# Performance work log

Hardware: AMD Instinct MI355X
Metric: run time of the kernel (lower is better)

The kernel has to match this reference:

```python
import jax, jax.numpy as jnp
import numpy as np

N_AGENTS, N_ENEMIES, N_ACTIONS = 8, 8, 14
ALLY_F, ENEMY_F = 8, 6
EMBED, RNN, HYPEMB, HYPHID = 32, 64, 64, 64
STATE_DIM = N_AGENTS * ALLY_F + N_ENEMIES * ENEMY_F + N_AGENTS * N_ACTIONS  # 224


def setup_inputs() -> dict:
    key = jax.random.key(0)
    ks = jax.random.split(key, 16)
    b, t = 64, 256
    rn = lambda k, s, sc=0.05: jax.random.normal(k, s, jnp.float32) * sc
    return dict(
        qvals=rn(ks[0], (b, t, N_AGENTS), 1.0),
        states=rn(ks[1], (b, t, STATE_DIM), 1.0),
        hidden_states=rn(ks[2], (b, t, N_AGENTS, RNN), 1.0),
        hw1_w=rn(ks[3], (RNN, EMBED)), hw1_b=jnp.zeros((EMBED,), jnp.float32),
        en_h1w=rn(ks[4], (ENEMY_F, HYPHID)), en_h1b=jnp.zeros((HYPHID,), jnp.float32),
        en_h2w=rn(ks[5], (HYPHID, ENEMY_F * HYPEMB)), en_h2b=jnp.zeros((ENEMY_F * HYPEMB,), jnp.float32),
        en_bias=jnp.zeros((1, HYPEMB), jnp.float32),
        al_h1w=rn(ks[6], (ALLY_F, HYPHID)), al_h1b=jnp.zeros((HYPHID,), jnp.float32),
        al_h2w=rn(ks[7], (HYPHID, ALLY_F * HYPEMB)), al_h2b=jnp.zeros((ALLY_F * HYPEMB,), jnp.float32),
        al_bias=jnp.zeros((1, HYPEMB), jnp.float32),
        act_w=rn(ks[8], (N_ACTIONS, HYPEMB)), act_b=jnp.zeros((HYPEMB,), jnp.float32),
        hb1_w=rn(ks[9], (HYPEMB, EMBED)), hb1_b=jnp.zeros((EMBED,), jnp.float32),
        hw2_w=rn(ks[10], (HYPEMB, EMBED)), hw2_b=jnp.zeros((EMBED,), jnp.float32),
        hb2_w=rn(ks[11], (HYPEMB, 1)), hb2_b=jnp.zeros((1,), jnp.float32),
    )


def _hyperlinear(x, h1w, h1b, h2w, h2b, bias, din, dout):
    # hypernet MLP -> per-sample weight matrix [rows, din, dout]
    h = jax.nn.relu(x @ h1w + h1b)
    W = (h @ h2w + h2b).reshape(-1, din, dout)
    return jnp.einsum('bi,bio->bo', x, W) + bias


def reference(qvals, states, hidden_states, hw1_w, hw1_b,
              en_h1w, en_h1b, en_h2w, en_h2b, en_bias,
              al_h1w, al_h1b, al_h2w, al_h2b, al_bias,
              act_w, act_b, hb1_w, hb1_b, hw2_w, hw2_b, hb2_w, hb2_b):
    b, t, _ = qvals.shape
    BT = b * t
    s = states.reshape(BT, STATE_DIM)
    ally = s[:, :N_AGENTS * ALLY_F].reshape(-1, ALLY_F)                # [BT*A, 8]
    enemy = s[:, N_AGENTS * ALLY_F:N_AGENTS * ALLY_F + N_ENEMIES * ENEMY_F].reshape(-1, ENEMY_F)
    actions = s[:, N_AGENTS * ALLY_F + N_ENEMIES * ENEMY_F:].reshape(BT, N_AGENTS, N_ACTIONS)

    embed_ally = _hyperlinear(ally, al_h1w, al_h1b, al_h2w, al_h2b, al_bias,
                              ALLY_F, HYPEMB).reshape(BT, N_AGENTS, HYPEMB).mean(axis=1)
    embed_enemy = _hyperlinear(enemy, en_h1w, en_h1b, en_h2w, en_h2b, en_bias,
                               ENEMY_F, HYPEMB).reshape(BT, N_ENEMIES, HYPEMB).mean(axis=1)
    embed_action = (actions @ act_w + act_b).mean(axis=1)
    se = jax.nn.relu(embed_ally + embed_enemy + embed_action)          # [BT, HYPEMB]

    w1 = jax.nn.softmax((hidden_states @ hw1_w + hw1_b).reshape(BT, N_AGENTS, EMBED), axis=1)
    b1 = (se @ hb1_w + hb1_b).reshape(BT, 1, EMBED)
    w2 = jnp.abs(se @ hw2_w + hw2_b).reshape(BT, EMBED, 1)
    b2 = (se @ hb2_w + hb2_b).reshape(BT, 1, 1)

    q = qvals.reshape(BT, 1, N_AGENTS)
    hidden = jax.nn.elu(jnp.matmul(q, w1) + b1)                        # [BT, 1, EMBED]
    y = jnp.matmul(hidden, w2) + b2                                    # [BT, 1, 1]
    return y.reshape(b, t, 1)
```

## Files before the change

kernel.cpp:

```cpp
#include <hip/hip_runtime.h>
#include <hip/hip_bf16.h>
#include <stdint.h>

typedef unsigned short u16t;
typedef float f32x4 __attribute__((ext_vector_type(4)));
typedef short bf16x8 __attribute__((ext_vector_type(8)));

#define SDIM 224

__device__ __forceinline__ float lo16(uint32_t w) { union { uint32_t u; float f; } v; v.u = w << 16; return v.f; }
__device__ __forceinline__ uint32_t f2bf(float f) {
    union { float f; uint32_t u; } v; v.f = f;
    return (v.u + 0x7FFFu + ((v.u >> 16) & 1u)) >> 16;
}

__global__ void prep_wt_kernel(const float* __restrict__ h2wA, const float* __restrict__ h2wB,
                               const float* __restrict__ hb1w, const float* __restrict__ hw2w,
                               const float* __restrict__ hw1w,
                               u16t* __restrict__ wtA, u16t* __restrict__ wtB,
                               u16t* __restrict__ wt2, u16t* __restrict__ wtM)
{
    const int t0 = blockIdx.x * 256 + threadIdx.x, stride = gridDim.x * 256;
    for (int e = t0; e < 32768; e += stride) {
        int j = e & 7, n = (e >> 3) & 63, kb = e >> 9;
        int k = kb * 8 + j, h = k & 63, i = k >> 6;
        wtA[e] = (u16t)f2bf(h2wA[h * 512 + i * 64 + n]);
    }
    for (int e = t0; e < 24576; e += stride) {
        int j = e & 7, n = (e >> 3) & 63, kb = e >> 9;
        int k = kb * 8 + j, h = k & 63, i = k >> 6;
        wtB[e] = (u16t)f2bf(h2wB[h * 384 + i * 64 + n]);
    }
    for (int e = t0; e < 4096; e += stride) {
        int j = e & 7, n = (e >> 3) & 63, kb = e >> 9;
        int k = kb * 8 + j;
        float v = (n < 32) ? hb1w[k * 32 + n] : hw2w[k * 32 + (n - 32)];
        wt2[e] = (u16t)f2bf(v);
    }
    for (int e = t0; e < 2048; e += stride) {
        int j = e & 7, n = (e >> 3) & 31, kb = e >> 8;
        int k = kb * 8 + j;
        wtM[e] = (u16t)f2bf(hw1w[k * 32 + n]);
    }
}

template<int DIN>
__device__ __forceinline__ void stage1_psum(const float (*s_x)[SDIM], u16t* s_psum, int KP,
                                            const float* s_h1w, const float* s_h1b,
                                            float (*s_xsum)[8], int wave, int lane, int foff)
{
    float w1r[DIN];
#pragma unroll
    for (int i = 0; i < DIN; ++i) w1r[i] = s_h1w[i * 64 + lane];
    const float b1r = s_h1b[lane];
    for (int ss = 0; ss < 4; ++ss) {
        const int s = wave * 4 + ss;
        const float* xr = &s_x[s][foff];
        float ps[DIN], xs[DIN];
#pragma unroll
        for (int i = 0; i < DIN; ++i) { ps[i] = 0.f; xs[i] = 0.f; }
#pragma unroll
        for (int a = 0; a < 8; ++a) {
            float x[DIN];
            if constexpr (DIN == 8) {
                float4 v0 = *(const float4*)&xr[a * 8];
                float4 v1 = *(const float4*)&xr[a * 8 + 4];
                x[0] = v0.x; x[1] = v0.y; x[2] = v0.z; x[3] = v0.w;
                x[4] = v1.x; x[5] = v1.y; x[6] = v1.z; x[7] = v1.w;
            } else {
                float2 v0 = *(const float2*)&xr[a * 6];
                float2 v1 = *(const float2*)&xr[a * 6 + 2];
                float2 v2 = *(const float2*)&xr[a * 6 + 4];
                x[0] = v0.x; x[1] = v0.y; x[2] = v1.x; x[3] = v1.y; x[4] = v2.x; x[5] = v2.y;
            }
            float hacc = b1r;
#pragma unroll
            for (int i = 0; i < DIN; ++i) hacc += x[i] * w1r[i];
            hacc = fmaxf(hacc, 0.f);
#pragma unroll
            for (int i = 0; i < DIN; ++i) { ps[i] += hacc * x[i]; xs[i] += x[i]; }
        }
#pragma unroll
        for (int i = 0; i < DIN; ++i) s_psum[s * KP + i * 64 + lane] = (u16t)f2bf(ps[i]);
        if (lane == 0) {
#pragma unroll
            for (int i = 0; i < DIN; ++i) s_xsum[s][i] = xs[i];
        }
    }
}

__global__ __launch_bounds__(256, 2)
void fused_mixer(const float* __restrict__ qvals, const float* __restrict__ states,
                 const float* __restrict__ hs,
                 const float* __restrict__ al_h1w, const float* __restrict__ al_h1b,
                 const float* __restrict__ al_h2b, const float* __restrict__ al_bias,
                 const float* __restrict__ en_h1w, const float* __restrict__ en_h1b,
                 const float* __restrict__ en_h2b, const float* __restrict__ en_bias,
                 const float* __restrict__ act_w, const float* __restrict__ act_b,
                 const float* __restrict__ hb1_b, const float* __restrict__ hw2_b,
                 const float* __restrict__ hw1_b, const float* __restrict__ hb2_w,
                 const float* __restrict__ hb2_b,
                 const u16t* __restrict__ wtA, const u16t* __restrict__ wtB,
                 const u16t* __restrict__ wt2, const u16t* __restrict__ wtM,
                 float* __restrict__ out)
{
    __shared__ __align__(16) float s_x[16][SDIM];
    __shared__ __align__(16) char  s_union[128 * 72 * 2];
    __shared__ __align__(16) u16t  s_se[16 * 72];
    __shared__ float s_b1w2[16][64];
    __shared__ float s_b2[16];
    __shared__ float s_q[128];
    __shared__ float s_am[16][14];
    __shared__ float s_xsum[16][8];
    __shared__ float s_h1wA[512], s_h2bA[512];
    __shared__ float s_h1wB[384], s_h2bB[384];
    __shared__ float s_actw[896];
    __shared__ float s_h1bA[64], s_h1bB[64], s_biasA[64], s_biasB[64], s_actb[64], s_hb2w[64];
    __shared__ float s_b1b[32], s_w2b[32], s_w1b[32];
    __shared__ float s_hb2b;

    const int tid  = threadIdx.x;
    const int wave = tid >> 6;
    const int lane = tid & 63;
    const int lr = lane & 15, lg = lane >> 4;
    const int sbase = blockIdx.x * 16;

    float4 hsr[8];
    {
        const float4* hsv = (const float4*)(hs + (size_t)sbase * 512);
#pragma unroll
        for (int i = 0; i < 8; ++i) hsr[i] = hsv[i * 256 + tid];
    }
    if (tid < 128) s_q[tid] = qvals[(size_t)sbase * 8 + tid];

    for (int i = tid; i < 16 * 56; i += 256) {
        int s = i / 56, c = i - s * 56;
        *(float4*)&s_x[s][c * 4] = *(const float4*)(states + (size_t)(sbase + s) * SDIM + c * 4);
    }
    for (int i = tid; i < 512; i += 256) { s_h1wA[i] = al_h1w[i]; s_h2bA[i] = al_h2b[i]; }
    for (int i = tid; i < 384; i += 256) { s_h1wB[i] = en_h1w[i]; s_h2bB[i] = en_h2b[i]; }
    for (int i = tid; i < 896; i += 256) s_actw[i] = act_w[i];
    if (tid < 64) {
        s_h1bA[tid] = al_h1b[tid]; s_h1bB[tid] = en_h1b[tid];
        s_biasA[tid] = al_bias[tid]; s_biasB[tid] = en_bias[tid];
        s_actb[tid] = act_b[tid]; s_hb2w[tid] = hb2_w[tid];
    }
    if (tid >= 64 && tid < 96)  s_b1b[tid - 64] = hb1_b[tid - 64];
    if (tid >= 96 && tid < 128) s_w2b[tid - 96] = hw2_b[tid - 96];
    if (tid >= 128 && tid < 160) s_w1b[tid - 128] = hw1_b[tid - 128];
    if (tid == 160) s_hb2b = hb2_b[0];
    __syncthreads();

    u16t* s_psum = (u16t*)s_union;
    constexpr int KPA = 520, KPB = 392;

    stage1_psum<8>(s_x, s_psum, KPA, s_h1wA, s_h1bA, s_xsum, wave, lane, 0);
    for (int i = tid; i < 224; i += 256) {
        int s = i / 14, j = i - s * 14;
        float a = 0.f;
#pragma unroll
        for (int aa = 0; aa < 8; ++aa) a += s_x[s][112 + aa * 14 + j];
        s_am[s][j] = a * 0.125f;
    }
    __syncthreads();

    const int n0 = wave * 16;
    const int o  = n0 + lr;
    float e[4];
    {
        f32x4 acc = {0.f, 0.f, 0.f, 0.f};
        const u16t* arow = &s_psum[lr * KPA + lg * 8];
        const bf16x8* wt8 = (const bf16x8*)wtA;
#pragma unroll 4
        for (int kk = 0; kk < 512; kk += 32) {
            bf16x8 av = *(const bf16x8*)(arow + kk);
            bf16x8 bv = wt8[((kk >> 3) + lg) * 64 + o];
            acc = __builtin_amdgcn_mfma_f32_16x16x32_bf16(av, bv, acc, 0, 0, 0);
        }
#pragma unroll
        for (int j = 0; j < 4; ++j) {
            const int row = lg * 4 + j;
            float hb = 0.f;
#pragma unroll
            for (int i = 0; i < 8; ++i) hb += s_xsum[row][i] * s_h2bA[i * 64 + o];
            e[j] = (acc[j] + hb) * 0.125f + s_biasA[o];
        }
    }
    __syncthreads();

    stage1_psum<6>(s_x, s_psum, KPB, s_h1wB, s_h1bB, s_xsum, wave, lane, 64);
    __syncthreads();

    {
        f32x4 acc = {0.f, 0.f, 0.f, 0.f};
        const u16t* arow = &s_psum[lr * KPB + lg * 8];
        const bf16x8* wt8 = (const bf16x8*)wtB;
#pragma unroll 4
        for (int kk = 0; kk < 384; kk += 32) {
            bf16x8 av = *(const bf16x8*)(arow + kk);
            bf16x8 bv = wt8[((kk >> 3) + lg) * 64 + o];
            acc = __builtin_amdgcn_mfma_f32_16x16x32_bf16(av, bv, acc, 0, 0, 0);
        }
#pragma unroll
        for (int j = 0; j < 4; ++j) {
            const int row = lg * 4 + j;
            float hb = 0.f;
#pragma unroll
            for (int i = 0; i < 6; ++i) hb += s_xsum[row][i] * s_h2bB[i * 64 + o];
            float se = e[j] + (acc[j] + hb) * 0.125f + s_biasB[o] + s_actb[o];
#pragma unroll
            for (int j2 = 0; j2 < 14; ++j2) se += s_am[row][j2] * s_actw[j2 * 64 + o];
            se = fmaxf(se, 0.f);
            s_se[row * 72 + o] = (u16t)f2bf(se);
        }
    }
    __syncthreads();

    u16t* s_hs = (u16t*)s_union;
    {
#pragma unroll
        for (int i = 0; i < 8; ++i) {
            const int idx = i * 256 + tid;
            const int row = idx >> 4, c4 = idx & 15;
            uint2 p;
            p.x = f2bf(hsr[i].x) | (f2bf(hsr[i].y) << 16);
            p.y = f2bf(hsr[i].z) | (f2bf(hsr[i].w) << 16);
            *(uint2*)&s_hs[row * 72 + c4 * 4] = p;
        }
    }
    {
        f32x4 acc = {0.f, 0.f, 0.f, 0.f};
        const bf16x8* wt8 = (const bf16x8*)wt2;
#pragma unroll
        for (int ks = 0; ks < 2; ++ks) {
            bf16x8 av = *(const bf16x8*)&s_se[lr * 72 + ks * 32 + lg * 8];
            bf16x8 bv = wt8[(ks * 4 + lg) * 64 + o];
            acc = __builtin_amdgcn_mfma_f32_16x16x32_bf16(av, bv, acc, 0, 0, 0);
        }
#pragma unroll
        for (int j = 0; j < 4; ++j) {
            const int row = lg * 4 + j;
            float v = acc[j] + ((o < 32) ? s_b1b[o] : s_w2b[o - 32]);
            if (o >= 32) v = fabsf(v);
            s_b1w2[row][o] = v;
        }
    }
    {
        const int smp = wave * 4 + lg;
        float p = 0.f;
#pragma unroll
        for (int c = 0; c < 4; ++c) {
            const int oo = c * 16 + lr;
            p += lo16((uint32_t)s_se[smp * 72 + oo]) * s_hb2w[oo];
        }
        p += __shfl_xor(p, 1); p += __shfl_xor(p, 2);
        p += __shfl_xor(p, 4); p += __shfl_xor(p, 8);
        if (lr == 0) s_b2[smp] = p + s_hb2b;
    }
    __syncthreads();

    bf16x8 bfr[2][2];
    {
        const bf16x8* wtm8 = (const bf16x8*)wtM;
#pragma unroll
        for (int n = 0; n < 2; ++n)
#pragma unroll
            for (int ks = 0; ks < 2; ++ks)
                bfr[n][ks] = wtm8[(ks * 4 + lg) * 32 + n * 16 + lr];
    }
    const float zb0 = s_w1b[lr], zb1 = s_w1b[16 + lr];

    for (int t = wave * 2; t < wave * 2 + 2; ++t) {
        f32x4 d0 = {0.f, 0.f, 0.f, 0.f}, d1 = {0.f, 0.f, 0.f, 0.f};
#pragma unroll
        for (int ks = 0; ks < 2; ++ks) {
            bf16x8 av = *(const bf16x8*)&s_hs[(t * 16 + lr) * 72 + ks * 32 + lg * 8];
            d0 = __builtin_amdgcn_mfma_f32_16x16x32_bf16(av, bfr[0][ks], d0, 0, 0, 0);
            d1 = __builtin_amdgcn_mfma_f32_16x16x32_bf16(av, bfr[1][ks], d1, 0, 0, 0);
        }
        const int sloc = t * 2 + (lg >> 1);
        float z0[4], z1[4];
#pragma unroll
        for (int j = 0; j < 4; ++j) { z0[j] = d0[j] + zb0; z1[j] = d1[j] + zb1; }
        float m0 = fmaxf(fmaxf(z0[0], z0[1]), fmaxf(z0[2], z0[3]));
        float m1 = fmaxf(fmaxf(z1[0], z1[1]), fmaxf(z1[2], z1[3]));
        m0 = fmaxf(m0, __shfl_xor(m0, 16));
        m1 = fmaxf(m1, __shfl_xor(m1, 16));
        float qa[4];
        {
            float4 qv = *(const float4*)&s_q[sloc * 8 + (lg & 1) * 4];
            qa[0] = qv.x; qa[1] = qv.y; qa[2] = qv.z; qa[3] = qv.w;
        }
        float s0 = 0.f, s1 = 0.f, hp0 = 0.f, hp1 = 0.f;
#pragma unroll
        for (int j = 0; j < 4; ++j) {
            float e0 = __expf(z0[j] - m0), e1 = __expf(z1[j] - m1);
            s0 += e0; s1 += e1;
            hp0 += qa[j] * e0; hp1 += qa[j] * e1;
        }
        s0  += __shfl_xor(s0, 16);  s1  += __shfl_xor(s1, 16);
        hp0 += __shfl_xor(hp0, 16); hp1 += __shfl_xor(hp1, 16);

        const float b1_0 = s_b1w2[sloc][lr],      b1_1 = s_b1w2[sloc][16 + lr];
        const float w2_0 = s_b1w2[sloc][32 + lr], w2_1 = s_b1w2[sloc][48 + lr];
        float h0 = hp0 / s0 + b1_0; h0 = (h0 > 0.f) ? h0 : (__expf(h0) - 1.f);
        float h1 = hp1 / s1 + b1_1; h1 = (h1 > 0.f) ? h1 : (__expf(h1) - 1.f);
        float yp = h0 * w2_0 + h1 * w2_1;
        yp += __shfl_xor(yp, 1); yp += __shfl_xor(yp, 2);
        yp += __shfl_xor(yp, 4); yp += __shfl_xor(yp, 8);
        if (lr == 0 && (lg & 1) == 0) out[sbase + sloc] = yp + s_b2[sloc];
    }
}

extern "C" void kernel_launch(void* const* d_in, const int* in_sizes, int n_in,
                              void* d_out, int out_size, void* d_ws, size_t ws_size,
                              hipStream_t stream) {
    const float* qvals   = (const float*)d_in[0];
    const float* states  = (const float*)d_in[1];
    const float* hstates = (const float*)d_in[2];
    const float* hw1_w   = (const float*)d_in[3];
    const float* hw1_b   = (const float*)d_in[4];
    const float* en_h1w  = (const float*)d_in[5];
    const float* en_h1b  = (const float*)d_in[6];
    const float* en_h2w  = (const float*)d_in[7];
    const float* en_h2b  = (const float*)d_in[8];
    const float* en_bias = (const float*)d_in[9];
    const float* al_h1w  = (const float*)d_in[10];
    const float* al_h1b  = (const float*)d_in[11];
    const float* al_h2w  = (const float*)d_in[12];
    const float* al_h2b  = (const float*)d_in[13];
    const float* al_bias = (const float*)d_in[14];
    const float* act_w   = (const float*)d_in[15];
    const float* act_b   = (const float*)d_in[16];
    const float* hb1_w   = (const float*)d_in[17];
    const float* hb1_b   = (const float*)d_in[18];
    const float* hw2_w   = (const float*)d_in[19];
    const float* hw2_b   = (const float*)d_in[20];
    const float* hb2_w   = (const float*)d_in[21];
    const float* hb2_b   = (const float*)d_in[22];

    u16t* wtA = (u16t*)d_ws;
    u16t* wtB = wtA + 32768;
    u16t* wt2 = wtA + 57344;
    u16t* wtM = wtA + 61440;

    prep_wt_kernel<<<64, 256, 0, stream>>>(al_h2w, en_h2w, hb1_w, hw2_w, hw1_w, wtA, wtB, wt2, wtM);
    fused_mixer<<<1024, 256, 0, stream>>>(qvals, states, hstates,
                                          al_h1w, al_h1b, al_h2b, al_bias,
                                          en_h1w, en_h1b, en_h2b, en_bias,
                                          act_w, act_b, hb1_b, hw2_b, hw1_b, hb2_w, hb2_b,
                                          wtA, wtB, wt2, wtM, (float*)d_out);
}
```

Measured before the change: 41.41 us.

## Store states tile as bf16 in LDS and move small weights to registers

```diff
diff --git a/kernel.cpp b/kernel.cpp
--- a/kernel.cpp
+++ b/kernel.cpp
@@ -9,6 +9,7 @@
 #define SDIM 224
 
 __device__ __forceinline__ float lo16(uint32_t w) { union { uint32_t u; float f; } v; v.u = w << 16; return v.f; }
+__device__ __forceinline__ float hi16(uint32_t w) { union { uint32_t u; float f; } v; v.u = w & 0xFFFF0000u; return v.f; }
 __device__ __forceinline__ uint32_t f2bf(float f) {
     union { float f; uint32_t u; } v; v.f = f;
     return (v.u + 0x7FFFu + ((v.u >> 16) & 1u)) >> 16;
@@ -45,7 +46,7 @@
 }
 
 template<int DIN>
-__device__ __forceinline__ void stage1_psum(const float (*s_x)[SDIM], u16t* s_psum, int KP,
+__device__ __forceinline__ void stage1_psum(const u16t (*s_xb)[SDIM], u16t* s_psum, int KP,
                                             const float* s_h1w, const float* s_h1b,
                                             float (*s_xsum)[8], int wave, int lane, int foff)
 {
@@ -55,7 +56,6 @@
     const float b1r = s_h1b[lane];
     for (int ss = 0; ss < 4; ++ss) {
         const int s = wave * 4 + ss;
-        const float* xr = &s_x[s][foff];
         float ps[DIN], xs[DIN];
 #pragma unroll
         for (int i = 0; i < DIN; ++i) { ps[i] = 0.f; xs[i] = 0.f; }
@@ -63,15 +63,16 @@
         for (int a = 0; a < 8; ++a) {
             float x[DIN];
             if constexpr (DIN == 8) {
-                float4 v0 = *(const float4*)&xr[a * 8];
-                float4 v1 = *(const float4*)&xr[a * 8 + 4];
-                x[0] = v0.x; x[1] = v0.y; x[2] = v0.z; x[3] = v0.w;
-                x[4] = v1.x; x[5] = v1.y; x[6] = v1.z; x[7] = v1.w;
+                uint4 v = *(const uint4*)&s_xb[s][a * 8];
+                x[0] = lo16(v.x); x[1] = hi16(v.x); x[2] = lo16(v.y); x[3] = hi16(v.y);
+                x[4] = lo16(v.z); x[5] = hi16(v.z); x[6] = lo16(v.w); x[7] = hi16(v.w);
             } else {
-                float2 v0 = *(const float2*)&xr[a * 6];
-                float2 v1 = *(const float2*)&xr[a * 6 + 2];
-                float2 v2 = *(const float2*)&xr[a * 6 + 4];
-                x[0] = v0.x; x[1] = v0.y; x[2] = v1.x; x[3] = v1.y; x[4] = v2.x; x[5] = v2.y;
+                const u16t* p = &s_xb[s][foff + a * 6];
+                uint32_t w0 = *(const uint32_t*)(p);
+                uint32_t w1 = *(const uint32_t*)(p + 2);
+                uint32_t w2 = *(const uint32_t*)(p + 4);
+                x[0] = lo16(w0); x[1] = hi16(w0); x[2] = lo16(w1);
+                x[3] = hi16(w1); x[4] = lo16(w2); x[5] = hi16(w2);
             }
             float hacc = b1r;
 #pragma unroll
@@ -89,7 +90,7 @@
     }
 }
 
-__global__ __launch_bounds__(256, 2)
+__global__ __launch_bounds__(256, 4)
 void fused_mixer(const float* __restrict__ qvals, const float* __restrict__ states,
                  const float* __restrict__ hs,
                  const float* __restrict__ al_h1w, const float* __restrict__ al_h1b,
@@ -104,17 +105,15 @@
                  const u16t* __restrict__ wt2, const u16t* __restrict__ wtM,
                  float* __restrict__ out)
 {
-    __shared__ __align__(16) float s_x[16][SDIM];
     __shared__ __align__(16) char  s_union[128 * 72 * 2];
+    __shared__ __align__(16) u16t  s_xb[16][SDIM];
     __shared__ __align__(16) u16t  s_se[16 * 72];
     __shared__ float s_b1w2[16][64];
     __shared__ float s_b2[16];
     __shared__ float s_q[128];
     __shared__ float s_am[16][14];
     __shared__ float s_xsum[16][8];
-    __shared__ float s_h1wA[512], s_h2bA[512];
-    __shared__ float s_h1wB[384], s_h2bB[384];
-    __shared__ float s_actw[896];
+    __shared__ float s_h1wA[512], s_h1wB[384];
     __shared__ float s_h1bA[64], s_h1bB[64], s_biasA[64], s_biasB[64], s_actb[64], s_hb2w[64];
     __shared__ float s_b1b[32], s_w2b[32], s_w1b[32];
     __shared__ float s_hb2b;
@@ -124,6 +123,7 @@
     const int lane = tid & 63;
     const int lr = lane & 15, lg = lane >> 4;
     const int sbase = blockIdx.x * 16;
+    const int o = wave * 16 + lr;
 
     float4 hsr[8];
     {
@@ -131,15 +131,28 @@
 #pragma unroll
         for (int i = 0; i < 8; ++i) hsr[i] = hsv[i * 256 + tid];
     }
+    float h2bA_r[8], h2bB_r[6], actw_r[14];
+#pragma unroll
+    for (int i = 0; i < 8; ++i) h2bA_r[i] = al_h2b[i * 64 + o];
+#pragma unroll
+    for (int i = 0; i < 6; ++i) h2bB_r[i] = en_h2b[i * 64 + o];
+#pragma unroll
+    for (int j = 0; j < 14; ++j) actw_r[j] = act_w[j * 64 + o];
     if (tid < 128) s_q[tid] = qvals[(size_t)sbase * 8 + tid];
 
-    for (int i = tid; i < 16 * 56; i += 256) {
-        int s = i / 56, c = i - s * 56;
-        *(float4*)&s_x[s][c * 4] = *(const float4*)(states + (size_t)(sbase + s) * SDIM + c * 4);
-    }
-    for (int i = tid; i < 512; i += 256) { s_h1wA[i] = al_h1w[i]; s_h2bA[i] = al_h2b[i]; }
-    for (int i = tid; i < 384; i += 256) { s_h1wB[i] = en_h1w[i]; s_h2bB[i] = en_h2b[i]; }
-    for (int i = tid; i < 896; i += 256) s_actw[i] = act_w[i];
+    for (int i = tid; i < 16 * 28; i += 256) {
+        int s = i / 28, c = i - s * 28;
+        const float4* sp = (const float4*)(states + (size_t)(sbase + s) * SDIM + c * 8);
+        float4 v0 = sp[0], v1 = sp[1];
+        uint4 p;
+        p.x = f2bf(v0.x) | (f2bf(v0.y) << 16);
+        p.y = f2bf(v0.z) | (f2bf(v0.w) << 16);
+        p.z = f2bf(v1.x) | (f2bf(v1.y) << 16);
+        p.w = f2bf(v1.z) | (f2bf(v1.w) << 16);
+        *(uint4*)&s_xb[s][c * 8] = p;
+    }
+    for (int i = tid; i < 512; i += 256) s_h1wA[i] = al_h1w[i];
+    for (int i = tid; i < 384; i += 256) s_h1wB[i] = en_h1w[i];
     if (tid < 64) {
         s_h1bA[tid] = al_h1b[tid]; s_h1bB[tid] = en_h1b[tid];
         s_biasA[tid] = al_bias[tid]; s_biasB[tid] = en_bias[tid];
@@ -154,18 +167,16 @@
     u16t* s_psum = (u16t*)s_union;
     constexpr int KPA = 520, KPB = 392;
 
-    stage1_psum<8>(s_x, s_psum, KPA, s_h1wA, s_h1bA, s_xsum, wave, lane, 0);
+    stage1_psum<8>(s_xb, s_psum, KPA, s_h1wA, s_h1bA, s_xsum, wave, lane, 0);
     for (int i = tid; i < 224; i += 256) {
         int s = i / 14, j = i - s * 14;
         float a = 0.f;
 #pragma unroll
-        for (int aa = 0; aa < 8; ++aa) a += s_x[s][112 + aa * 14 + j];
+        for (int aa = 0; aa < 8; ++aa) a += lo16((uint32_t)s_xb[s][112 + aa * 14 + j]);
         s_am[s][j] = a * 0.125f;
     }
     __syncthreads();
 
-    const int n0 = wave * 16;
-    const int o  = n0 + lr;
     float e[4];
     {
         f32x4 acc = {0.f, 0.f, 0.f, 0.f};
@@ -182,13 +193,13 @@
             const int row = lg * 4 + j;
             float hb = 0.f;
 #pragma unroll
-            for (int i = 0; i < 8; ++i) hb += s_xsum[row][i] * s_h2bA[i * 64 + o];
+            for (int i = 0; i < 8; ++i) hb += s_xsum[row][i] * h2bA_r[i];
             e[j] = (acc[j] + hb) * 0.125f + s_biasA[o];
         }
     }
     __syncthreads();
 
-    stage1_psum<6>(s_x, s_psum, KPB, s_h1wB, s_h1bB, s_xsum, wave, lane, 64);
+    stage1_psum<6>(s_xb, s_psum, KPB, s_h1wB, s_h1bB, s_xsum, wave, lane, 64);
     __syncthreads();
 
     {
@@ -206,10 +217,10 @@
             const int row = lg * 4 + j;
             float hb = 0.f;
 #pragma unroll
-            for (int i = 0; i < 6; ++i) hb += s_xsum[row][i] * s_h2bB[i * 64 + o];
+            for (int i = 0; i < 6; ++i) hb += s_xsum[row][i] * h2bB_r[i];
             float se = e[j] + (acc[j] + hb) * 0.125f + s_biasB[o] + s_actb[o];
 #pragma unroll
-            for (int j2 = 0; j2 < 14; ++j2) se += s_am[row][j2] * s_actw[j2 * 64 + o];
+            for (int j2 = 0; j2 < 14; ++j2) se += s_am[row][j2] * actw_r[j2];
             se = fmaxf(se, 0.f);
             s_se[row * 72 + o] = (u16t)f2bf(se);
         }
```

Result: slower. 51.18 us (+23.6%).
